# Kernel optimization log

Measured on AMD Instinct MI355X. Metric: run time of the kernel, lower is better.

Reference implementation:

```python
import jax, jax.numpy as jnp
import numpy as np

NEG = -9e15  # mask value used by dense GAT implementations
BN_EPS = 1e-5


def gat_layer(x, W, a_src, a_dst, adj_mask):
    # Dense-adjacency GAT layer (pyGAT GraphAttentionLayer math).
    Wh = x @ W                                              # [N, H]
    e = jax.nn.leaky_relu(
        (Wh @ a_src)[:, None] + (Wh @ a_dst)[None, :], 0.2)  # [N, N]
    scores = jnp.where(adj_mask, e, NEG)
    att = jax.nn.softmax(scores, axis=1)                    # scatter-softmax over neighbors
    return att @ Wh                                         # [N, H]


def batchnorm(h, gamma, beta):
    # BatchNorm1d in training mode: biased batch stats over the node axis.
    mu = h.mean(axis=0)
    var = h.var(axis=0)
    return gamma * (h - mu) * jax.lax.rsqrt(var + BN_EPS) + beta


def setup_inputs() -> dict:
    key = jax.random.key(0)
    ks = jax.random.split(key, 8)
    N, F, H = 4096, 512, 256
    x = jax.random.normal(ks[0], (N, F), dtype=jnp.float32)
    adj = jax.random.randint(ks[1], (N, N), 0, 2, dtype=jnp.int32)
    W1 = jax.random.normal(ks[2], (F, H), dtype=jnp.float32) / np.sqrt(F)
    a1_src = jax.random.normal(ks[3], (H,), dtype=jnp.float32) / np.sqrt(H)
    a1_dst = jax.random.normal(ks[4], (H,), dtype=jnp.float32) / np.sqrt(H)
    W2 = jax.random.normal(ks[5], (H, H), dtype=jnp.float32) / np.sqrt(H)
    a2_src = jax.random.normal(ks[6], (H,), dtype=jnp.float32) / np.sqrt(H)
    a2_dst = jax.random.normal(ks[7], (H,), dtype=jnp.float32) / np.sqrt(H)
    return {
        "x": x, "adj": adj,
        "W1": W1, "a1_src": a1_src, "a1_dst": a1_dst,
        "gamma1": jnp.ones((H,), jnp.float32), "beta1": jnp.zeros((H,), jnp.float32),
        "W2": W2, "a2_src": a2_src, "a2_dst": a2_dst,
        "gamma2": jnp.ones((H,), jnp.float32), "beta2": jnp.zeros((H,), jnp.float32),
    }


def reference(x, adj, W1, a1_src, a1_dst, gamma1, beta1,
              W2, a2_src, a2_dst, gamma2, beta2):
    adj_mask = adj > 0
    h = jax.nn.relu(gat_layer(x, W1, a1_src, a1_dst, adj_mask))
    h = batchnorm(h, gamma1, beta1)
    # dropout is identity at inference time (deterministic reference)
    h = jax.nn.relu(gat_layer(h, W2, a2_src, a2_dst, adj_mask))
    h = batchnorm(h, gamma2, beta2)
    return h
```

## Files before the change

### kernel.cpp

```cpp
#include <hip/hip_runtime.h>

#define LOG2E 1.4426950408889634f

typedef unsigned long long u64;
typedef unsigned int uint;
typedef unsigned short ushort_t;
typedef __attribute__((ext_vector_type(8))) short short8;
typedef __attribute__((ext_vector_type(4))) float floatx4;
typedef __attribute__((ext_vector_type(4))) int intx4;
typedef __attribute__((ext_vector_type(4))) unsigned short ushort4v;

#define GN 4096
#define GH 256
#define KZ 8
#define KSTEPS 16

__device__ __forceinline__ ushort_t f2bf(float f){
  uint u = __float_as_uint(f);
  u += 0x7FFFu + ((u >> 16) & 1u);
  return (ushort_t)(u >> 16);
}
__device__ __forceinline__ float bf2f(ushort_t h){
  return __uint_as_float(((uint)h) << 16);
}
__device__ __forceinline__ float exp2_(float x){
#if __has_builtin(__builtin_amdgcn_exp2f)
  return __builtin_amdgcn_exp2f(x);
#else
  return exp2f(x);
#endif
}

__global__ __launch_bounds__(256) void prep(const int* __restrict__ adj,
                                            u64* __restrict__ mask,
                                            const float* __restrict__ W1,
                                            ushort_t* __restrict__ W1h,
                                            ushort_t* __restrict__ W1l,
                                            const float* __restrict__ W2,
                                            ushort_t* __restrict__ W2h,
                                            ushort_t* __restrict__ W2l){
  __shared__ union {
    unsigned char nib[4][1024];
    ushort_t tt[2][32][33];
  } sh;
  const int t = threadIdx.x;
  if (blockIdx.x < 1024){
    const int r0 = blockIdx.x * 4;
    const int* base = adj + (size_t)r0 * GN;
    #pragma unroll
    for (int i = 0; i < 16; ++i){
      int c = i * 256 + t;
      intx4 v = *(const intx4*)(base + c * 4);
      uint n = (uint)(v[0] > 0) | ((uint)(v[1] > 0) << 1) |
               ((uint)(v[2] > 0) << 2) | ((uint)(v[3] > 0) << 3);
      sh.nib[c >> 10][c & 1023] = (unsigned char)n;
    }
    __syncthreads();
    {
      int r = t >> 6, wi = t & 63;
      const u64* p = (const u64*)sh.nib[r];
      u64 x0 = p[wi * 2], x1 = p[wi * 2 + 1];
      auto comp = [](u64 x)->u64{
        x = (x | (x >> 4))  & 0x00FF00FF00FF00FFULL;
        x = (x | (x >> 8))  & 0x0000FFFF0000FFFFULL;
        x = (x | (x >> 16)) & 0x00000000FFFFFFFFULL;
        return x;
      };
      mask[(size_t)(r0 + r) * 64 + wi] = comp(x0) | (comp(x1) << 32);
    }
    return;
  }
  int b = blockIdx.x - 1024;
  const float* in; ushort_t* hi; ushort_t* lo; int R, idx;
  if (b < 128){ in = W1; hi = W1h; lo = W1l; R = 512; idx = b; }
  else        { in = W2; hi = W2h; lo = W2l; R = 256; idx = b - 128; }
  const int C = GH;
  const int bx = idx & 7, by = idx >> 3;
  const int i0 = by * 32, j0 = bx * 32;
  const int r = t >> 3, c4 = (t & 7) * 4;
  floatx4 v = *(const floatx4*)(in + (size_t)(i0 + r) * C + j0 + c4);
  #pragma unroll
  for (int e = 0; e < 4; ++e){
    ushort_t h = f2bf(v[e]);
    sh.tt[0][r][c4 + e] = h;
    sh.tt[1][r][c4 + e] = f2bf(v[e] - bf2f(h));
  }
  __syncthreads();
  ushort4v oh, ol;
  #pragma unroll
  for (int e = 0; e < 4; ++e){ oh[e] = sh.tt[0][c4 + e][r]; ol[e] = sh.tt[1][c4 + e][r]; }
  *(ushort4v*)(hi + (size_t)(j0 + r) * R + i0 + c4) = oh;
  *(ushort4v*)(lo + (size_t)(j0 + r) * R + i0 + c4) = ol;
}

template<bool BN>
__global__ __launch_bounds__(256) void gemm_split(const float* __restrict__ A,
                                                  const ushort_t* __restrict__ BThi,
                                                  const ushort_t* __restrict__ BTlo,
                                                  const float* __restrict__ bnsc,
                                                  const float* __restrict__ bnbi,
                                                  float* __restrict__ Cf, int K){
  __shared__ short8 AhiV[32 * 8];
  __shared__ short8 AloV[32 * 8];
  __shared__ short8 BhiV[64 * 8];
  __shared__ short8 BloV[64 * 8];
  char* Ahi = (char*)AhiV; char* Alo = (char*)AloV;
  char* Bhi = (char*)BhiV; char* Blo = (char*)BloV;
  const int tid = threadIdx.x;
  const int i0 = blockIdx.y * 32, n0 = blockIdx.x * 64;
  const int lane = tid & 63, wave = tid >> 6;
  const int wr = wave & 1, wc = wave >> 1;
  const int l15 = lane & 15, lhi = lane >> 4;
  const int rs = tid >> 3, ch = tid & 7;
  floatx4 acc[2] = {};
  for (int kb = 0; kb < K; kb += 64){
    {
      int r = rs;
      floatx4 f0 = *(const floatx4*)(A + (size_t)(i0 + r) * K + kb + ch * 8);
      floatx4 f1 = *(const floatx4*)(A + (size_t)(i0 + r) * K + kb + ch * 8 + 4);
      if constexpr (BN){
        floatx4 sc0 = *(const floatx4*)(bnsc + kb + ch * 8);
        floatx4 sc1 = *(const floatx4*)(bnsc + kb + ch * 8 + 4);
        floatx4 bi0 = *(const floatx4*)(bnbi + kb + ch * 8);
        floatx4 bi1 = *(const floatx4*)(bnbi + kb + ch * 8 + 4);
        #pragma unroll
        for (int e = 0; e < 4; ++e){
          f0[e] = f0[e] * sc0[e] + bi0[e];
          f1[e] = f1[e] * sc1[e] + bi1[e];
        }
      }
      short8 ah, al;
      #pragma unroll
      for (int e = 0; e < 4; ++e){
        ushort_t h0 = f2bf(f0[e]); ah[e] = (short)h0; al[e] = (short)f2bf(f0[e] - bf2f(h0));
        ushort_t h1 = f2bf(f1[e]); ah[e+4] = (short)h1; al[e+4] = (short)f2bf(f1[e] - bf2f(h1));
      }
      const int sw = (ch * 16) ^ ((r & 7) << 4);
      *(short8*)(Ahi + r * 128 + sw) = ah;
      *(short8*)(Alo + r * 128 + sw) = al;
      #pragma unroll
      for (int q = 0; q < 2; ++q){
        int rb = rs + q * 32;
        const int swb = (ch * 16) ^ ((rb & 7) << 4);
        short8 bh = *(const short8*)(BThi + (size_t)(n0 + rb) * K + kb + ch * 8);
        short8 bl = *(const short8*)(BTlo + (size_t)(n0 + rb) * K + kb + ch * 8);
        *(short8*)(Bhi + rb * 128 + swb) = bh;
        *(short8*)(Blo + rb * 128 + swb) = bl;
      }
    }
    __syncthreads();
    #pragma unroll
    for (int kt = 0; kt < 2; ++kt){
      int klb = (kt * 32 + lhi * 8) * 2;
      int rowA = wr * 16 + l15;
      int swA = klb ^ ((rowA & 7) << 4);
      short8 ah = *(const short8*)(Ahi + rowA * 128 + swA);
      short8 al = *(const short8*)(Alo + rowA * 128 + swA);
      #pragma unroll
      for (int n = 0; n < 2; ++n){
        int rowB = wc * 32 + n * 16 + l15;
        int swB = klb ^ ((rowB & 7) << 4);
        short8 bh = *(const short8*)(Bhi + rowB * 128 + swB);
        short8 bl = *(const short8*)(Blo + rowB * 128 + swB);
        acc[n] = __builtin_amdgcn_mfma_f32_16x16x32_bf16(ah, bh, acc[n], 0, 0, 0);
        acc[n] = __builtin_amdgcn_mfma_f32_16x16x32_bf16(ah, bl, acc[n], 0, 0, 0);
        acc[n] = __builtin_amdgcn_mfma_f32_16x16x32_bf16(al, bh, acc[n], 0, 0, 0);
      }
    }
    __syncthreads();
  }
  #pragma unroll
  for (int rr = 0; rr < 4; ++rr){
    int row = i0 + wr * 16 + lhi * 4 + rr;
    #pragma unroll
    for (int n = 0; n < 2; ++n){
      int col = n0 + wc * 32 + n * 16 + l15;
      Cf[(size_t)row * GH + col] = acc[n][rr];
    }
  }
}

__global__ __launch_bounds__(256) void skthi(const float* __restrict__ Whf,
                                             const float* __restrict__ asrc,
                                             const float* __restrict__ adst,
                                             float* __restrict__ ss,
                                             float* __restrict__ sd,
                                             ushort_t* __restrict__ VTh){
  __shared__ ushort_t tile[256][36];
  const int tid = threadIdx.x;
  const int i0 = blockIdx.x * 32;
  const int r = tid >> 3, cg = tid & 7;
  float s = 0.f, d = 0.f;
  #pragma unroll
  for (int j = 0; j < 8; ++j){
    int col = j * 32 + cg * 4;
    floatx4 v = *(const floatx4*)(Whf + (size_t)(i0 + r) * GH + col);
    floatx4 s4 = *(const floatx4*)(asrc + col);
    floatx4 d4 = *(const floatx4*)(adst + col);
    #pragma unroll
    for (int e = 0; e < 4; ++e){
      s += v[e] * s4[e]; d += v[e] * d4[e];
      tile[col + e][r] = f2bf(v[e]);
    }
  }
  #pragma unroll
  for (int off = 1; off < 8; off <<= 1){
    s += __shfl_xor(s, off);
    d += __shfl_xor(d, off);
  }
  if (cg == 0){ ss[i0 + r] = s * LOG2E; sd[i0 + r] = d * LOG2E; }
  __syncthreads();
  const int rr4 = (tid & 7) * 4, cb = tid >> 3;
  #pragma unroll
  for (int ct = 0; ct < 8; ++ct){
    int col = ct * 32 + cb;
    ushort4v o = *(const ushort4v*)(&tile[col][rr4]);
    *(ushort4v*)(VTh + (size_t)col * GN + i0 + rr4) = o;
  }
}

__global__ __launch_bounds__(128) void gat_pv(const u64* __restrict__ mask,
                                              const float* __restrict__ ss,
                                              const float* __restrict__ sd,
                                              const ushort_t* __restrict__ VTh,
                                              float* __restrict__ partial,
                                              float* __restrict__ szb){
  __shared__ char Blds[20480];
  __shared__ char Plds[32 * 80];
  __shared__ float wsum[2][32];
  const int tid = threadIdx.x;
  const int lane = tid & 63, w = tid >> 6;
  const int l15 = lane & 15, lhi = lane >> 4;
  const int i0 = blockIdx.x * 32;
  const int kz = blockIdx.y;
  const int ch = tid & 3, c0 = tid >> 2;
  const int ncol0 = w * 128;

  const int prow = l15 + ((lhi & 1) << 4);
  const int row = i0 + prow;
  const float ssr = ss[row];
  const int kkb = w * 16 + ((lhi >> 1) << 3);

  u64 mw[8];
  {
    const u64* mr = mask + (size_t)row * 64 + kz * 8;
    #pragma unroll
    for (int q = 0; q < 8; ++q) mw[q] = mr[q];
  }

  floatx4 acc[2][8] = {};
  float srow = 0.f;
  short8 g[8];

  auto GLOAD = [&](int kb){
    const int kbase = (kz * KSTEPS + kb) * 32;
    #pragma unroll
    for (int i = 0; i < 8; ++i){
      int c = c0 + 32 * i;
      g[i] = *(const short8*)(VTh + (size_t)c * GN + kbase + ch * 8);
    }
  };
  auto SWRITE = [&](){
    #pragma unroll
    for (int i = 0; i < 8; ++i){
      int c = c0 + 32 * i;
      *(short8*)(Blds + c * 80 + ch * 16) = g[i];
    }
  };

  GLOAD(0); SWRITE(); __syncthreads();

  for (int kb = 0; kb < KSTEPS; ++kb){
    {
      const int kbase = (kz * KSTEPS + kb) * 32;
      floatx4 s0 = *(const floatx4*)(sd + kbase + kkb);
      floatx4 s1 = *(const floatx4*)(sd + kbase + kkb + 4);
      const int sh = ((kb & 1) << 5) + kkb;
      uint bits = (uint)(mw[kb >> 1] >> sh) & 0xffu;
      short8 pv;
      #pragma unroll
      for (int e = 0; e < 8; ++e){
        float sv = (e < 4) ? s0[e] : s1[e - 4];
        float t = ssr + sv;
        float lr = fmaxf(t, 0.2f * t);
        float p = exp2_(lr);
        p = ((bits >> e) & 1u) ? p : 0.0f;
        srow += p;
        pv[e] = (short)f2bf(p);
      }
      *(short8*)(Plds + prow * 80 + kkb * 2) = pv;
    }
    __syncthreads();

    if (kb + 1 < KSTEPS) GLOAD(kb + 1);

    short8 a0 = *(const short8*)(Plds + l15 * 80 + lhi * 16);
    short8 a1 = *(const short8*)(Plds + (l15 + 16) * 80 + lhi * 16);
    #pragma unroll
    for (int n = 0; n < 8; ++n){
      short8 b = *(const short8*)(Blds + (ncol0 + n * 16 + l15) * 80 + lhi * 16);
      acc[0][n] = __builtin_amdgcn_mfma_f32_16x16x32_bf16(a0, b, acc[0][n], 0, 0, 0);
      acc[1][n] = __builtin_amdgcn_mfma_f32_16x16x32_bf16(a1, b, acc[1][n], 0, 0, 0);
    }
    __syncthreads();
    if (kb + 1 < KSTEPS) SWRITE();
  }

  srow += __shfl_xor(srow, 32);
  if (lane < 32) wsum[w][prow] = srow;
  __syncthreads();
  if (w == 0 && lane < 32)
    szb[(size_t)kz * GN + i0 + lane] = wsum[0][lane] + wsum[1][lane];

  float* pout = partial + (size_t)kz * GN * GH;
  #pragma unroll
  for (int m = 0; m < 2; ++m){
    const int rbase = i0 + m * 16 + lhi * 4;
    #pragma unroll
    for (int n = 0; n < 8; ++n){
      int col = ncol0 + n * 16 + l15;
      #pragma unroll
      for (int rr = 0; rr < 4; ++rr)
        pout[(size_t)(rbase + rr) * GH + col] = acc[m][n][rr];
    }
  }
}

__global__ __launch_bounds__(256) void combine_colpart(const float* __restrict__ partial,
                                                       const float* __restrict__ szb,
                                                       float* __restrict__ outb,
                                                       float* __restrict__ part,
                                                       float* __restrict__ partm2){
  __shared__ float fl[4];
  __shared__ float sm[4][GH];
  const int tid = threadIdx.x;
  const int b = blockIdx.x;
  const int r0 = b * 4;
  if (tid < 4){
    int row = r0 + tid;
    float lsum = 0.f;
    #pragma unroll
    for (int z = 0; z < 8; ++z) lsum += szb[(size_t)z * GN + row];
    fl[tid] = lsum > 0.f ? 1.0f / lsum : 0.f;
  }
  __syncthreads();
  const int r = tid >> 6;
  const int c4 = (tid & 63) * 4;
  const size_t idx = (size_t)(r0 + r) * GH + c4;
  floatx4 x = {};
  #pragma unroll
  for (int z = 0; z < 8; ++z){
    floatx4 p = *(const floatx4*)(partial + (size_t)z * GN * GH + idx);
    #pragma unroll
    for (int e = 0; e < 4; ++e) x[e] += p[e];
  }
  const float linv = fl[r];
  #pragma unroll
  for (int e = 0; e < 4; ++e) x[e] = fmaxf(x[e] * linv, 0.0f);
  *(floatx4*)(outb + idx) = x;
  *(floatx4*)(&sm[r][c4]) = x;
  __syncthreads();
  if (tid < 64){
    const int cb = tid * 4;
    floatx4 v0 = *(const floatx4*)(&sm[0][cb]);
    floatx4 v1 = *(const floatx4*)(&sm[1][cb]);
    floatx4 v2 = *(const floatx4*)(&sm[2][cb]);
    floatx4 v3 = *(const floatx4*)(&sm[3][cb]);
    floatx4 s, m2;
    #pragma unroll
    for (int e = 0; e < 4; ++e){
      float sum = v0[e] + v1[e] + v2[e] + v3[e];
      float mu = sum * 0.25f;
      float d0 = v0[e]-mu, d1 = v1[e]-mu, d2 = v2[e]-mu, d3 = v3[e]-mu;
      s[e] = sum;
      m2[e] = d0*d0 + d1*d1 + d2*d2 + d3*d3;
    }
    *(floatx4*)(part + (size_t)b * GH + cb) = s;
    *(floatx4*)(partm2 + (size_t)b * GH + cb) = m2;
  }
}

__global__ __launch_bounds__(256) void colfin(const float* __restrict__ part,
                                              const float* __restrict__ partm2,
                                              const float* __restrict__ gamma,
                                              const float* __restrict__ beta,
                                              float* __restrict__ scale,
                                              float* __restrict__ bias){
  __shared__ double red[8][33];
  const int cl = threadIdx.x & 31, g = threadIdx.x >> 5;
  const int c = blockIdx.x * 32 + cl;
  double S = 0.0;
  for (int b = g * 128; b < g * 128 + 128; ++b) S += (double)part[(size_t)b * GH + c];
  red[g][cl] = S;
  __syncthreads();
  double mean = 0.0;
  #pragma unroll
  for (int q = 0; q < 8; ++q) mean += red[q][cl];
  mean *= (1.0 / 4096.0);
  double M2 = 0.0;
  for (int b = g * 128; b < g * 128 + 128; ++b){
    double mb = (double)part[(size_t)b * GH + c] * 0.25;
    double dd = mb - mean;
    M2 += (double)partm2[(size_t)b * GH + c] + 4.0 * dd * dd;
  }
  __syncthreads();
  red[g][cl] = M2;
  __syncthreads();
  if (g == 0){
    double M2t = 0.0;
    #pragma unroll
    for (int q = 0; q < 8; ++q) M2t += red[q][cl];
    double var = M2t * (1.0 / 4096.0);
    float sc = gamma[c] * (float)(1.0 / sqrt(var + 1e-5));
    scale[c] = sc;
    bias[c] = beta[c] - (float)mean * sc;
  }
}

__global__ __launch_bounds__(256) void bnapply(const float* __restrict__ outb,
                                               const float* __restrict__ scale,
                                               const float* __restrict__ bias,
                                               float* __restrict__ dst){
  const int base = (blockIdx.x * 256 + threadIdx.x) * 4;
  const int c = base & (GH - 1);
  floatx4 v = *(const floatx4*)(outb + base);
  floatx4 s = *(const floatx4*)(scale + c);
  floatx4 b = *(const floatx4*)(bias + c);
  #pragma unroll
  for (int e = 0; e < 4; ++e) v[e] = v[e] * s[e] + b[e];
  *(floatx4*)(dst + base) = v;
}

extern "C" void kernel_launch(void* const* d_in, const int* in_sizes, int n_in,
                              void* d_out, int out_size, void* d_ws, size_t ws_size,
                              hipStream_t stream) {
  const float* x      = (const float*)d_in[0];
  const int*   adj    = (const int*)d_in[1];
  const float* W1     = (const float*)d_in[2];
  const float* a1s    = (const float*)d_in[3];
  const float* a1d    = (const float*)d_in[4];
  const float* g1     = (const float*)d_in[5];
  const float* b1     = (const float*)d_in[6];
  const float* W2     = (const float*)d_in[7];
  const float* a2s    = (const float*)d_in[8];
  const float* a2d    = (const float*)d_in[9];
  const float* g2     = (const float*)d_in[10];
  const float* b2     = (const float*)d_in[11];

  char* w = (char*)d_ws;
  auto alloc = [&](size_t bytes){ void* p = (void*)w; w += (bytes + 255) & ~(size_t)255; return p; };
  u64*      mask   = (u64*)alloc((size_t)GN * 64 * 8);
  ushort_t* W1Th   = (ushort_t*)alloc((size_t)GH * 512 * 2);
  ushort_t* W1Tl   = (ushort_t*)alloc((size_t)GH * 512 * 2);
  ushort_t* W2Th   = (ushort_t*)alloc((size_t)GH * GH * 2);
  ushort_t* W2Tl   = (ushort_t*)alloc((size_t)GH * GH * 2);
  float*    Whf    = (float*)alloc((size_t)GN * GH * 4);
  ushort_t* VThb   = (ushort_t*)alloc((size_t)GH * GN * 2);
  float*    outb   = (float*)alloc((size_t)GN * GH * 4);
  float*    partial= (float*)alloc((size_t)KZ * GN * GH * 4);
  float*    ssb    = (float*)alloc(GN * 4);
  float*    sdb    = (float*)alloc(GN * 4);
  float*    szb    = (float*)alloc((size_t)KZ * GN * 4);
  float*    part   = (float*)alloc((size_t)1024 * GH * 4);
  float*    partm2 = (float*)alloc((size_t)1024 * GH * 4);
  float*    scale  = (float*)alloc(GH * 4);
  float*    bias   = (float*)alloc(GH * 4);

  prep<<<1024 + 192, 256, 0, stream>>>(adj, mask, W1, W1Th, W1Tl, W2, W2Th, W2Tl);

  gemm_split<false><<<dim3(4, 128), 256, 0, stream>>>(x, W1Th, W1Tl, nullptr, nullptr, Whf, 512);
  skthi<<<128, 256, 0, stream>>>(Whf, a1s, a1d, ssb, sdb, VThb);
  gat_pv<<<dim3(GN/32, KZ), 128, 0, stream>>>(mask, ssb, sdb, VThb, partial, szb);
  combine_colpart<<<1024, 256, 0, stream>>>(partial, szb, outb, part, partm2);
  colfin<<<8, 256, 0, stream>>>(part, partm2, g1, b1, scale, bias);

  gemm_split<true><<<dim3(4, 128), 256, 0, stream>>>(outb, W2Th, W2Tl, scale, bias, Whf, 256);
  skthi<<<128, 256, 0, stream>>>(Whf, a2s, a2d, ssb, sdb, VThb);
  gat_pv<<<dim3(GN/32, KZ), 128, 0, stream>>>(mask, ssb, sdb, VThb, partial, szb);
  combine_colpart<<<1024, 256, 0, stream>>>(partial, szb, outb, part, partm2);
  colfin<<<8, 256, 0, stream>>>(part, partm2, g2, b2, scale, bias);
  bnapply<<<1024, 256, 0, stream>>>(outb, scale, bias, (float*)d_out);
}
```

Baseline: 137.8 us.

## Fuse attention-score dot products and bf16 transpose into GEMM epilogue

The GEMM epilogue now converts its accumulator tile to bf16, writes it directly in the transposed VTh layout, and computes per-row partial dot products with a_src/a_dst for its 64-column slice. A small sfin kernel then sums the four column-block partials into the score vectors. This removes the fp32 Whf round trip through global memory and the separate skthi transpose kernel. In exchange it adds a cross-lane reduction, an extra launch, and narrow 8-byte strided stores into VTh.

```diff
diff --git a/kernel.cpp b/kernel.cpp
--- a/kernel.cpp
+++ b/kernel.cpp
@@ -99,11 +99,16 @@
                                                   const ushort_t* __restrict__ BTlo,
                                                   const float* __restrict__ bnsc,
                                                   const float* __restrict__ bnbi,
-                                                  float* __restrict__ Cf, int K){
+                                                  const float* __restrict__ as,
+                                                  const float* __restrict__ ad,
+                                                  ushort_t* __restrict__ VTh,
+                                                  float* __restrict__ spart,
+                                                  int K){
   __shared__ short8 AhiV[32 * 8];
   __shared__ short8 AloV[32 * 8];
   __shared__ short8 BhiV[64 * 8];
   __shared__ short8 BloV[64 * 8];
+  __shared__ float red[32][2][2];
   char* Ahi = (char*)AhiV; char* Alo = (char*)AloV;
   char* Bhi = (char*)BhiV; char* Blo = (char*)BloV;
   const int tid = threadIdx.x;
@@ -169,54 +174,58 @@
     }
     __syncthreads();
   }
-  #pragma unroll
-  for (int rr = 0; rr < 4; ++rr){
-    int row = i0 + wr * 16 + lhi * 4 + rr;
-    #pragma unroll
-    for (int n = 0; n < 2; ++n){
-      int col = n0 + wc * 32 + n * 16 + l15;
-      Cf[(size_t)row * GH + col] = acc[n][rr];
-    }
-  }
-}
-
-__global__ __launch_bounds__(256) void skthi(const float* __restrict__ Whf,
-                                             const float* __restrict__ asrc,
-                                             const float* __restrict__ adst,
-                                             float* __restrict__ ss,
-                                             float* __restrict__ sd,
-                                             ushort_t* __restrict__ VTh){
-  __shared__ ushort_t tile[256][36];
-  const int tid = threadIdx.x;
-  const int i0 = blockIdx.x * 32;
-  const int r = tid >> 3, cg = tid & 7;
+  float sp[4] = {0.f, 0.f, 0.f, 0.f};
+  float dp[4] = {0.f, 0.f, 0.f, 0.f};
+  #pragma unroll
+  for (int n = 0; n < 2; ++n){
+    int col = n0 + wc * 32 + n * 16 + l15;
+    float asv = as[col], adv = ad[col];
+    ushort4v o;
+    #pragma unroll
+    for (int rr = 0; rr < 4; ++rr){
+      float v = acc[n][rr];
+      o[rr] = f2bf(v);
+      sp[rr] += v * asv;
+      dp[rr] += v * adv;
+    }
+    *(ushort4v*)(VTh + (size_t)col * GN + i0 + wr * 16 + lhi * 4) = o;
+  }
+  #pragma unroll
+  for (int off = 1; off < 16; off <<= 1){
+    #pragma unroll
+    for (int rr = 0; rr < 4; ++rr){
+      sp[rr] += __shfl_xor(sp[rr], off);
+      dp[rr] += __shfl_xor(dp[rr], off);
+    }
+  }
+  if (l15 == 0){
+    #pragma unroll
+    for (int rr = 0; rr < 4; ++rr){
+      int r = wr * 16 + lhi * 4 + rr;
+      red[r][wc][0] = sp[rr];
+      red[r][wc][1] = dp[rr];
+    }
+  }
+  __syncthreads();
+  if (tid < 64){
+    int r = tid >> 1, sel = tid & 1;
+    float v = red[r][0][sel] + red[r][1][sel];
+    spart[((size_t)sel * 4 + blockIdx.x) * GN + i0 + r] = v;
+  }
+}
+
+__global__ __launch_bounds__(256) void sfin(const float* __restrict__ spart,
+                                            float* __restrict__ ss,
+                                            float* __restrict__ sd){
+  const int i = blockIdx.x * 256 + threadIdx.x;
   float s = 0.f, d = 0.f;
   #pragma unroll
-  for (int j = 0; j < 8; ++j){
-    int col = j * 32 + cg * 4;
-    floatx4 v = *(const floatx4*)(Whf + (size_t)(i0 + r) * GH + col);
-    floatx4 s4 = *(const floatx4*)(asrc + col);
-    floatx4 d4 = *(const floatx4*)(adst + col);
-    #pragma unroll
-    for (int e = 0; e < 4; ++e){
-      s += v[e] * s4[e]; d += v[e] * d4[e];
-      tile[col + e][r] = f2bf(v[e]);
-    }
-  }
-  #pragma unroll
-  for (int off = 1; off < 8; off <<= 1){
-    s += __shfl_xor(s, off);
-    d += __shfl_xor(d, off);
-  }
-  if (cg == 0){ ss[i0 + r] = s * LOG2E; sd[i0 + r] = d * LOG2E; }
-  __syncthreads();
-  const int rr4 = (tid & 7) * 4, cb = tid >> 3;
-  #pragma unroll
-  for (int ct = 0; ct < 8; ++ct){
-    int col = ct * 32 + cb;
-    ushort4v o = *(const ushort4v*)(&tile[col][rr4]);
-    *(ushort4v*)(VTh + (size_t)col * GN + i0 + rr4) = o;
-  }
+  for (int q = 0; q < 4; ++q){
+    s += spart[(size_t)q * GN + i];
+    d += spart[(size_t)(4 + q) * GN + i];
+  }
+  ss[i] = s * LOG2E;
+  sd[i] = d * LOG2E;
 }
 
 __global__ __launch_bounds__(128) void gat_pv(const u64* __restrict__ mask,
@@ -454,10 +463,10 @@
   ushort_t* W1Tl   = (ushort_t*)alloc((size_t)GH * 512 * 2);
   ushort_t* W2Th   = (ushort_t*)alloc((size_t)GH * GH * 2);
   ushort_t* W2Tl   = (ushort_t*)alloc((size_t)GH * GH * 2);
-  float*    Whf    = (float*)alloc((size_t)GN * GH * 4);
   ushort_t* VThb   = (ushort_t*)alloc((size_t)GH * GN * 2);
   float*    outb   = (float*)alloc((size_t)GN * GH * 4);
   float*    partial= (float*)alloc((size_t)KZ * GN * GH * 4);
+  float*    spart  = (float*)alloc((size_t)2 * 4 * GN * 4);
   float*    ssb    = (float*)alloc(GN * 4);
   float*    sdb    = (float*)alloc(GN * 4);
   float*    szb    = (float*)alloc((size_t)KZ * GN * 4);
@@ -468,14 +477,16 @@
 
   prep<<<1024 + 192, 256, 0, stream>>>(adj, mask, W1, W1Th, W1Tl, W2, W2Th, W2Tl);
 
-  gemm_split<false><<<dim3(4, 128), 256, 0, stream>>>(x, W1Th, W1Tl, nullptr, nullptr, Whf, 512);
-  skthi<<<128, 256, 0, stream>>>(Whf, a1s, a1d, ssb, sdb, VThb);
+  gemm_split<false><<<dim3(4, 128), 256, 0, stream>>>(x, W1Th, W1Tl, nullptr, nullptr,
+                                                      a1s, a1d, VThb, spart, 512);
+  sfin<<<GN/256, 256, 0, stream>>>(spart, ssb, sdb);
   gat_pv<<<dim3(GN/32, KZ), 128, 0, stream>>>(mask, ssb, sdb, VThb, partial, szb);
   combine_colpart<<<1024, 256, 0, stream>>>(partial, szb, outb, part, partm2);
   colfin<<<8, 256, 0, stream>>>(part, partm2, g1, b1, scale, bias);
 
-  gemm_split<true><<<dim3(4, 128), 256, 0, stream>>>(outb, W2Th, W2Tl, scale, bias, Whf, 256);
-  skthi<<<128, 256, 0, stream>>>(Whf, a2s, a2d, ssb, sdb, VThb);
+  gemm_split<true><<<dim3(4, 128), 256, 0, stream>>>(outb, W2Th, W2Tl, scale, bias,
+                                                     a2s, a2d, VThb, spart, 256);
+  sfin<<<GN/256, 256, 0, stream>>>(spart, ssb, sdb);
   gat_pv<<<dim3(GN/32, KZ), 128, 0, stream>>>(mask, ssb, sdb, VThb, partial, szb);
   combine_colpart<<<1024, 256, 0, stream>>>(partial, szb, outb, part, partm2);
   colfin<<<8, 256, 0, stream>>>(part, partm2, g2, b2, scale, bias);
```

After: 139.5 us. About the same (+1.2%).
